# Kernel tuning notes

Hardware: AMD Instinct MI355X
Metric: run time of the kernel (lower is better)

The kernel has to match this reference:

```python
import jax, jax.numpy as jnp
import numpy as np

B, S, D, H, F = 4, 2048, 1024, 16, 4096
HD = D // H
NEG = -2.0 ** 32
EPS = 1e-5


def _gelu(x):
    return x * 0.5 * (1.0 + jax.scipy.special.erf(x / jnp.sqrt(2.0).astype(x.dtype)))


def _layernorm(x, scale, offset):
    mu = jnp.mean(x, axis=-1, keepdims=True)
    var = jnp.mean(jnp.square(x - mu), axis=-1, keepdims=True)
    return (x - mu) * jax.lax.rsqrt(var + EPS) * scale + offset


def setup_inputs() -> dict:
    key = jax.random.key(0)
    ks = jax.random.split(key, 12)
    s = 0.02
    return {
        "x": jax.random.normal(ks[0], (B, S, D), jnp.float32),
        "mask": jnp.zeros((B, S), jnp.int32),  # 1 = masked-out (padding)
        "Wq": jax.random.normal(ks[1], (D, D), jnp.float32) * s,
        "bq": jnp.zeros((D,), jnp.float32),
        "Wk": jax.random.normal(ks[2], (D, D), jnp.float32) * s,
        "bk": jnp.zeros((D,), jnp.float32),
        "Wv": jax.random.normal(ks[3], (D, D), jnp.float32) * s,
        "bv": jnp.zeros((D,), jnp.float32),
        "Wo": jax.random.normal(ks[4], (D, D), jnp.float32) * s,
        "bo": jnp.zeros((D,), jnp.float32),
        "ln1_s": jnp.ones((D,), jnp.float32),
        "ln1_b": jnp.zeros((D,), jnp.float32),
        "W1": jax.random.normal(ks[5], (D, F), jnp.float32) * s,
        "b1": jnp.zeros((F,), jnp.float32),
        "W2": jax.random.normal(ks[6], (F, D), jnp.float32) * s,
        "b2": jnp.zeros((D,), jnp.float32),
        "ln2_s": jnp.ones((D,), jnp.float32),
        "ln2_b": jnp.zeros((D,), jnp.float32),
    }


def reference(x, mask, Wq, bq, Wk, bk, Wv, bv, Wo, bo, ln1_s, ln1_b,
              W1, b1, W2, b2, ln2_s, ln2_b):
    b, s, d = x.shape
    q = (x @ Wq + bq).reshape(b, s, H, HD)
    k = (x @ Wk + bk).reshape(b, s, H, HD)
    v = (x @ Wv + bv).reshape(b, s, H, HD)
    logits = jnp.einsum('btnh,bsnh->bnts', q, k) / jnp.sqrt(jnp.float32(HD))
    logits = logits + (mask.astype(jnp.float32) * NEG)[:, None, None, :]
    attn = jax.nn.softmax(logits, axis=-1)
    ctx = jnp.einsum('bsnh,bnts->btnh', v, attn).reshape(b, s, d)
    attn_out = ctx @ Wo + bo
    h = _layernorm(attn_out + x, ln1_s, ln1_b)
    mlp = _gelu(h @ W1 + b1) @ W2 + b2
    return _layernorm(mlp + h, ln2_s, ln2_b)
```

## Files before the change

kernel.cpp:

```cpp
#include <hip/hip_runtime.h>
#include <hip/hip_bf16.h>

typedef __attribute__((ext_vector_type(8))) short short8;
typedef __attribute__((ext_vector_type(4))) short s16x4;
typedef __attribute__((ext_vector_type(4))) float f32x4;
typedef unsigned short u16;

#define DEV __device__ __forceinline__
#define MFMA32(a, b, c) __builtin_amdgcn_mfma_f32_16x16x32_bf16(a, b, c, 0, 0, 0)
#define MFMA16(a, b, c) __builtin_amdgcn_mfma_f32_16x16x16bf16_1k(a, b, c, 0, 0, 0)

DEV u16 f2b(float f) {
    __hip_bfloat16 h = __float2bfloat16(f);
    return __builtin_bit_cast(unsigned short, h);
}

DEV float max3f(float a, float b, float c) {
    float d;
    asm("v_max3_f32 %0, %1, %2, %3" : "=v"(d) : "v"(a), "v"(b), "v"(c));
    return d;
}

DEV void gl_lds16(const u16* g, u16* l) {
    __builtin_amdgcn_global_load_lds((const unsigned int*)g, (unsigned int*)l, 16, 0, 0);
}

__global__ __launch_bounds__(256) void cast_bf16(const float* __restrict__ in, u16* __restrict__ out, int n) {
    int i = (blockIdx.x * 256 + threadIdx.x) * 4;
    if (i < n) {
        float4 v = *(const float4*)(in + i);
        ushort4 o;
        o.x = f2b(v.x); o.y = f2b(v.y); o.z = f2b(v.z); o.w = f2b(v.w);
        *(ushort4*)(out + i) = o;
    }
}

__global__ __launch_bounds__(256) void transpose_cast(const float* __restrict__ in, u16* __restrict__ out,
                                                      int R, int C) {
    __shared__ float t[32][33];
    int bx = blockIdx.x * 32;
    int by = blockIdx.y * 32;
    int tx = threadIdx.x, ty = threadIdx.y;
#pragma unroll
    for (int i = 0; i < 32; i += 8) t[ty + i][tx] = in[(size_t)(by + ty + i) * C + bx + tx];
    __syncthreads();
#pragma unroll
    for (int i = 0; i < 32; i += 8) out[(size_t)(bx + ty + i) * R + by + tx] = f2b(t[tx][ty + i]);
}

__global__ __launch_bounds__(256) void pack_bias(const float* __restrict__ bq, const float* __restrict__ bk,
                                                 const float* __restrict__ bv, const float* __restrict__ bo,
                                                 const float* __restrict__ b1, const float* __restrict__ b2,
                                                 float* __restrict__ out) {
    int i = blockIdx.x * 256 + threadIdx.x;
    if (i >= 9216) return;
    float v;
    if (i < 1024) v = bq[i];
    else if (i < 2048) v = bk[i - 1024];
    else if (i < 3072) v = bv[i - 2048];
    else if (i < 4096) v = bo[i - 3072];
    else if (i < 8192) v = b1[i - 4096];
    else v = b2[i - 8192];
    out[i] = v;
}

template <bool GELU, bool BF16OUT, bool RESID>
__global__ __launch_bounds__(256) void gemm_bt(const u16* __restrict__ A, const u16* __restrict__ B,
                                               const float* __restrict__ bias, float* __restrict__ cf,
                                               u16* __restrict__ cb, const float* __restrict__ res,
                                               int M, int N, int K) {
    __shared__ __align__(16) u16 As[128 * 32];
    __shared__ __align__(16) u16 Bs[128 * 32];
    const int tid = threadIdx.x;
    const int wid = tid >> 6, lane = tid & 63;
    const int wr = wid >> 1, wc = wid & 1;
    const int m0 = blockIdx.x * 128, n0 = blockIdx.y * 128;
    const int r16 = lane & 15, g = lane >> 4;
    const int lrow = lane >> 2, lk = (lane & 3) * 8;

    f32x4 acc[4][4];
#pragma unroll
    for (int i = 0; i < 4; i++)
#pragma unroll
        for (int j = 0; j < 4; j++) acc[i][j] = (f32x4){0.f, 0.f, 0.f, 0.f};

    const u16* ga = A + (size_t)(m0 + wid * 32 + lrow) * K + lk;
    const u16* gb = B + (size_t)(n0 + wid * 32 + lrow) * K + lk;
    u16* lA0 = &As[(wid * 32) * 32];
    u16* lA1 = &As[(wid * 32 + 16) * 32];
    u16* lB0 = &Bs[(wid * 32) * 32];
    u16* lB1 = &Bs[(wid * 32 + 16) * 32];

    for (int kt = 0; kt < K; kt += 32) {
        gl_lds16(ga + kt, lA0);
        gl_lds16(ga + (size_t)16 * K + kt, lA1);
        gl_lds16(gb + kt, lB0);
        gl_lds16(gb + (size_t)16 * K + kt, lB1);
        __syncthreads();
        short8 af[4], bfr[4];
#pragma unroll
        for (int i = 0; i < 4; i++) af[i] = *(const short8*)&As[(wr * 64 + i * 16 + r16) * 32 + g * 8];
#pragma unroll
        for (int j = 0; j < 4; j++) bfr[j] = *(const short8*)&Bs[(wc * 64 + j * 16 + r16) * 32 + g * 8];
#pragma unroll
        for (int i = 0; i < 4; i++)
#pragma unroll
            for (int j = 0; j < 4; j++) acc[i][j] = MFMA32(af[i], bfr[j], acc[i][j]);
        __syncthreads();
    }

#pragma unroll
    for (int i = 0; i < 4; i++) {
#pragma unroll
        for (int j = 0; j < 4; j++) {
#pragma unroll
            for (int r = 0; r < 4; r++) {
                int row = m0 + wr * 64 + i * 16 + g * 4 + r;
                int col = n0 + wc * 64 + j * 16 + r16;
                float v = acc[i][j][r] + bias[col];
                if (RESID) v += res[(size_t)row * N + col];
                if (GELU) v = 0.5f * v * (1.0f + erff(v * 0.70710678118654752f));
                if (BF16OUT) cb[(size_t)row * N + col] = f2b(v);
                else cf[(size_t)row * N + col] = v;
            }
        }
    }
}

__global__ __launch_bounds__(256, 4) void attn_kernel(const u16* __restrict__ qkv, const int* __restrict__ mask,
                                                      u16* __restrict__ ctx) {
    const int tid = threadIdx.x, wid = tid >> 6, lane = tid & 63;
    const int r16 = lane & 15, g = lane >> 4;
    const int h = blockIdx.y, b = blockIdx.z;
    const size_t baserow = (size_t)b * 2048;
    const int q0 = blockIdx.x * 128;

    __shared__ __align__(16) u16 Ks[64 * 64];
    __shared__ __align__(16) u16 Vs[64 * 64];
    __shared__ unsigned tflags_sh;

    const float SCALE = 0.18033688011112042f;
    const float MNEG = -6.196328018e9f;
    const s16x4 ONES = {(short)0x3F80, (short)0x3F80, (short)0x3F80, (short)0x3F80};

    short8 qfA0, qfA1, qfB0, qfB1;
    {
        const u16* qp = qkv + (baserow + q0 + wid * 32 + r16) * 3072 + h * 64 + g * 8;
        qfA0 = *(const short8*)qp;
        qfA1 = *(const short8*)(qp + 32);
        qfB0 = *(const short8*)(qp + (size_t)16 * 3072);
        qfB1 = *(const short8*)(qp + (size_t)16 * 3072 + 32);
    }

    if (tid == 0) tflags_sh = 0;
    __syncthreads();
    for (int r = 0; r < 8; ++r) {
        int v = mask[baserow + r * 256 + tid];
        unsigned long long bal = __ballot(v != 0);
        if (bal != 0 && lane == 0) atomicOr(&tflags_sh, 1u << (r * 4 + wid));
    }

    const int L = lane;
    const u16* kg0 = qkv + (baserow + wid * 16 + (L >> 3)) * 3072 + 1024 + h * 64 + ((L & 7) ^ (L >> 3)) * 8;
    const u16* kg1 = kg0 + (size_t)8 * 3072;
    u16* kl0 = &Ks[wid * 1024];
    u16* kl1 = &Ks[wid * 1024 + 512];
    const u16* vg0 = qkv + (baserow + wid * 16 + ((L & 31) >> 1)) * 3072 + 2048 + h * 64
                     + ((L >> 5) * 16 + (L & 1) * 8);
    const u16* vg1 = vg0 + 32;
    u16* vl0 = &Vs[wid * 1024];
    u16* vl1 = &Vs[wid * 1024 + 512];
    const unsigned vaddr = (unsigned)(unsigned long long)&Vs[0] + (unsigned)(r16 * 2 + g * 128);

    __syncthreads();
    const unsigned tfl = tflags_sh;

    f32x4 OtA[4], OtB[4];
#pragma unroll
    for (int dt = 0; dt < 4; dt++) { OtA[dt] = (f32x4){0.f, 0.f, 0.f, 0.f}; OtB[dt] = (f32x4){0.f, 0.f, 0.f, 0.f}; }
    f32x4 OsumA = (f32x4){0.f, 0.f, 0.f, 0.f}, OsumB = (f32x4){0.f, 0.f, 0.f, 0.f};
    float mrunA = -1e30f, mrunB = -1e30f;

    for (int t = 0; t < 32; ++t) {
        const int kt = t * 64;
        const size_t go = (size_t)kt * 3072;
        gl_lds16(kg0 + go, kl0);
        gl_lds16(kg1 + go, kl1);
        gl_lds16(vg0 + go, vl0);
        gl_lds16(vg1 + go, vl1);
        __syncthreads();

        f32x4 zA[4], zB[4];
        __builtin_amdgcn_s_setprio(1);
#pragma unroll
        for (int tt = 0; tt < 4; tt++) {
            const int row = tt * 16 + r16;
            const int swz = row & 7;
            short8 a0 = *(const short8*)&Ks[row * 64 + ((g ^ swz) * 8)];
            short8 a1 = *(const short8*)&Ks[row * 64 + (((4 + g) ^ swz) * 8)];
            f32x4 za = (f32x4){0.f, 0.f, 0.f, 0.f};
            za = MFMA32(a0, qfA0, za);
            za = MFMA32(a1, qfA1, za);
            zA[tt] = za;
            f32x4 zb = (f32x4){0.f, 0.f, 0.f, 0.f};
            zb = MFMA32(a0, qfB0, zb);
            zb = MFMA32(a1, qfB1, zb);
            zB[tt] = zb;
        }
        __builtin_amdgcn_s_setprio(0);

        float a0_ = max3f(zA[0][0], zA[0][1], zA[0][2]);
        float a1_ = max3f(zA[0][3], zA[1][0], zA[1][1]);
        float a2_ = max3f(zA[1][2], zA[1][3], zA[2][0]);
        float a3_ = max3f(zA[2][1], zA[2][2], zA[2][3]);
        float a4_ = max3f(zA[3][0], zA[3][1], zA[3][2]);
        float zmaxA = fmaxf(max3f(a0_, a1_, a2_), max3f(a3_, a4_, zA[3][3]));
        float b0_ = max3f(zB[0][0], zB[0][1], zB[0][2]);
        float b1_ = max3f(zB[0][3], zB[1][0], zB[1][1]);
        float b2_ = max3f(zB[1][2], zB[1][3], zB[2][0]);
        float b3_ = max3f(zB[2][1], zB[2][2], zB[2][3]);
        float b4_ = max3f(zB[3][0], zB[3][1], zB[3][2]);
        float zmaxB = fmaxf(max3f(b0_, b1_, b2_), max3f(b3_, b4_, zB[3][3]));
        zmaxA = fmaxf(zmaxA, __shfl_xor(zmaxA, 16));
        zmaxB = fmaxf(zmaxB, __shfl_xor(zmaxB, 16));
        zmaxA = fmaxf(zmaxA, __shfl_xor(zmaxA, 32));
        zmaxB = fmaxf(zmaxB, __shfl_xor(zmaxB, 32));
        float pmaxA = zmaxA * SCALE, pmaxB = zmaxB * SCALE;

        if (!__all(pmaxA - mrunA <= 11.5f)) {
            float mnew = fmaxf(mrunA, pmaxA);
            float alpha = exp2f(mrunA - mnew);
            mrunA = mnew;
            OsumA *= alpha;
#pragma unroll
            for (int dt = 0; dt < 4; dt++) OtA[dt] *= alpha;
        }
        if (!__all(pmaxB - mrunB <= 11.5f)) {
            float mnew = fmaxf(mrunB, pmaxB);
            float alpha = exp2f(mrunB - mnew);
            mrunB = mnew;
            OsumB *= alpha;
#pragma unroll
            for (int dt = 0; dt < 4; dt++) OtB[dt] *= alpha;
        }

        s16x4 pbA[4], pbB[4];
        const float negmA = -mrunA, negmB = -mrunB;
        if (__builtin_expect((tfl >> t) & 1u, 0)) {
            const int* mrow = mask + baserow + kt;
#pragma unroll
            for (int tt = 0; tt < 4; tt++) {
                float pa[4], pbv[4];
#pragma unroll
                for (int j = 0; j < 4; j++) {
                    float mbj = mrow[tt * 16 + g * 4 + j] ? MNEG : 0.0f;
                    pa[j] = exp2f(__builtin_fmaf(zA[tt][j], SCALE, mbj + negmA));
                    pbv[j] = exp2f(__builtin_fmaf(zB[tt][j], SCALE, mbj + negmB));
                }
                unsigned lo, hi;
                asm("v_cvt_pk_bf16_f32 %0, %1, %2" : "=v"(lo) : "v"(pa[0]), "v"(pa[1]));
                asm("v_cvt_pk_bf16_f32 %0, %1, %2" : "=v"(hi) : "v"(pa[2]), "v"(pa[3]));
                uint2 ua; ua.x = lo; ua.y = hi;
                pbA[tt] = __builtin_bit_cast(s16x4, ua);
                asm("v_cvt_pk_bf16_f32 %0, %1, %2" : "=v"(lo) : "v"(pbv[0]), "v"(pbv[1]));
                asm("v_cvt_pk_bf16_f32 %0, %1, %2" : "=v"(hi) : "v"(pbv[2]), "v"(pbv[3]));
                uint2 ub; ub.x = lo; ub.y = hi;
                pbB[tt] = __builtin_bit_cast(s16x4, ub);
            }
        } else {
#pragma unroll
            for (int tt = 0; tt < 4; tt++) {
                float pa0 = exp2f(__builtin_fmaf(zA[tt][0], SCALE, negmA));
                float pa1 = exp2f(__builtin_fmaf(zA[tt][1], SCALE, negmA));
                float pa2 = exp2f(__builtin_fmaf(zA[tt][2], SCALE, negmA));
                float pa3 = exp2f(__builtin_fmaf(zA[tt][3], SCALE, negmA));
                float pb0 = exp2f(__builtin_fmaf(zB[tt][0], SCALE, negmB));
                float pb1 = exp2f(__builtin_fmaf(zB[tt][1], SCALE, negmB));
                float pb2 = exp2f(__builtin_fmaf(zB[tt][2], SCALE, negmB));
                float pb3 = exp2f(__builtin_fmaf(zB[tt][3], SCALE, negmB));
                unsigned lo, hi;
                asm("v_cvt_pk_bf16_f32 %0, %1, %2" : "=v"(lo) : "v"(pa0), "v"(pa1));
                asm("v_cvt_pk_bf16_f32 %0, %1, %2" : "=v"(hi) : "v"(pa2), "v"(pa3));
                uint2 ua; ua.x = lo; ua.y = hi;
                pbA[tt] = __builtin_bit_cast(s16x4, ua);
                asm("v_cvt_pk_bf16_f32 %0, %1, %2" : "=v"(lo) : "v"(pb0), "v"(pb1));
                asm("v_cvt_pk_bf16_f32 %0, %1, %2" : "=v"(hi) : "v"(pb2), "v"(pb3));
                uint2 ub; ub.x = lo; ub.y = hi;
                pbB[tt] = __builtin_bit_cast(s16x4, ub);
            }
        }

        s16x4 vf[2][4];
#pragma unroll
        for (int dt = 0; dt < 4; dt++)
            asm volatile("ds_read_b64_tr_b16 %0, %1"
                         : "=v"(vf[0][dt]) : "v"(vaddr + (unsigned)(dt * 512)));
#pragma unroll
        for (int tt = 0; tt < 4; tt++) {
            if (tt < 3) {
#pragma unroll
                for (int dt = 0; dt < 4; dt++)
                    asm volatile("ds_read_b64_tr_b16 %0, %1"
                                 : "=v"(vf[(tt + 1) & 1][dt])
                                 : "v"(vaddr + (unsigned)(((tt + 1) * 4 + dt) * 512)));
                asm volatile("s_waitcnt lgkmcnt(4)" ::: "memory");
            } else {
                asm volatile("s_waitcnt lgkmcnt(0)" ::: "memory");
            }
            __builtin_amdgcn_sched_barrier(0);
            __builtin_amdgcn_s_setprio(1);
#pragma unroll
            for (int dt = 0; dt < 4; dt++) {
                OtA[dt] = MFMA16(vf[tt & 1][dt], pbA[tt], OtA[dt]);
                OtB[dt] = MFMA16(vf[tt & 1][dt], pbB[tt], OtB[dt]);
            }
            OsumA = MFMA16(ONES, pbA[tt], OsumA);
            OsumB = MFMA16(ONES, pbB[tt], OsumB);
            __builtin_amdgcn_s_setprio(0);
        }
        __syncthreads();
    }

    const float rlA = 1.0f / OsumA[0];
    const float rlB = 1.0f / OsumB[0];
    u16* cpA = ctx + (baserow + q0 + wid * 32 + r16) * 1024 + h * 64 + g * 4;
    u16* cpB = cpA + (size_t)16 * 1024;
#pragma unroll
    for (int dt = 0; dt < 4; dt++) {
        ushort4 oa, ob;
        oa.x = f2b(OtA[dt][0] * rlA); oa.y = f2b(OtA[dt][1] * rlA);
        oa.z = f2b(OtA[dt][2] * rlA); oa.w = f2b(OtA[dt][3] * rlA);
        ob.x = f2b(OtB[dt][0] * rlB); ob.y = f2b(OtB[dt][1] * rlB);
        ob.z = f2b(OtB[dt][2] * rlB); ob.w = f2b(OtB[dt][3] * rlB);
        *(ushort4*)(cpA + dt * 16) = oa;
        *(ushort4*)(cpB + dt * 16) = ob;
    }
}

__global__ __launch_bounds__(256) void ln_kernel(const float* __restrict__ a, const float* __restrict__ res,
                                                 const float* __restrict__ gamma, const float* __restrict__ beta,
                                                 float* __restrict__ outf, u16* __restrict__ outb) {
    const int row = blockIdx.x, tid = threadIdx.x;
    const size_t base = (size_t)row * 1024 + tid * 4;
    float4 va = *(const float4*)(a + base);
    float x0 = va.x, x1 = va.y, x2 = va.z, x3 = va.w;
    if (res) {
        float4 vr = *(const float4*)(res + base);
        x0 += vr.x; x1 += vr.y; x2 += vr.z; x3 += vr.w;
    }
    float s = x0 + x1 + x2 + x3;
    float ss = x0 * x0 + x1 * x1 + x2 * x2 + x3 * x3;
#pragma unroll
    for (int m = 1; m < 64; m <<= 1) { s += __shfl_xor(s, m, 64); ss += __shfl_xor(ss, m, 64); }
    __shared__ float red[8];
    if ((tid & 63) == 0) { red[tid >> 6] = s; red[4 + (tid >> 6)] = ss; }
    __syncthreads();
    s = red[0] + red[1] + red[2] + red[3];
    ss = red[4] + red[5] + red[6] + red[7];
    float mu = s * (1.0f / 1024.0f);
    float var = ss * (1.0f / 1024.0f) - mu * mu;
    float rstd = rsqrtf(var + 1e-5f);
    float4 g4 = *(const float4*)(gamma + tid * 4);
    float4 b4 = *(const float4*)(beta + tid * 4);
    float y0 = (x0 - mu) * rstd * g4.x + b4.x;
    float y1 = (x1 - mu) * rstd * g4.y + b4.y;
    float y2 = (x2 - mu) * rstd * g4.z + b4.z;
    float y3 = (x3 - mu) * rstd * g4.w + b4.w;
    *(float4*)(outf + base) = make_float4(y0, y1, y2, y3);
    if (outb) {
        ushort4 ob;
        ob.x = f2b(y0); ob.y = f2b(y1); ob.z = f2b(y2); ob.w = f2b(y3);
        *(ushort4*)(outb + base) = ob;
    }
}

extern "C" void kernel_launch(void* const* d_in, const int* in_sizes, int n_in, void* d_out, int out_size,
                              void* d_ws, size_t ws_size, hipStream_t stream) {
    const float* x = (const float*)d_in[0];
    const int* mask = (const int*)d_in[1];
    const float* Wq = (const float*)d_in[2];
    const float* bq = (const float*)d_in[3];
    const float* Wk = (const float*)d_in[4];
    const float* bk = (const float*)d_in[5];
    const float* Wv = (const float*)d_in[6];
    const float* bv = (const float*)d_in[7];
    const float* Wo = (const float*)d_in[8];
    const float* bo = (const float*)d_in[9];
    const float* ln1s = (const float*)d_in[10];
    const float* ln1b = (const float*)d_in[11];
    const float* W1 = (const float*)d_in[12];
    const float* b1 = (const float*)d_in[13];
    const float* W2 = (const float*)d_in[14];
    const float* b2 = (const float*)d_in[15];
    const float* ln2s = (const float*)d_in[16];
    const float* ln2b = (const float*)d_in[17];
    float* out = (float*)d_out;
    char* ws = (char*)d_ws;

    const size_t MB = 1024 * 1024;
    u16* XB = (u16*)(ws + 0);
    u16* WTq = (u16*)(ws + 16 * MB);
    u16* WTk = WTq + 1024 * 1024;
    u16* WTv = WTk + 1024 * 1024;
    u16* WTo = WTv + 1024 * 1024;
    u16* WT1 = WTo + 1024 * 1024;
    u16* WT2 = WT1 + 4096 * 1024;
    float* BIAS = (float*)(ws + 40 * MB);
    u16* QKV = (u16*)(ws + 41 * MB);
    u16* CTX = (u16*)(ws + 0);
    float* ATT = (float*)(ws + 41 * MB);
    float* Hbuf = (float*)(ws + 73 * MB);
    u16* HB = (u16*)(ws + 105 * MB);
    u16* MLP1 = (u16*)(ws + 121 * MB);
    float* MLP2 = (float*)(ws + 41 * MB);

    dim3 tb(32, 8);
    cast_bf16<<<8192, 256, 0, stream>>>(x, XB, 8192 * 1024);
    transpose_cast<<<dim3(32, 32), tb, 0, stream>>>(Wq, WTq, 1024, 1024);
    transpose_cast<<<dim3(32, 32), tb, 0, stream>>>(Wk, WTk, 1024, 1024);
    transpose_cast<<<dim3(32, 32), tb, 0, stream>>>(Wv, WTv, 1024, 1024);
    transpose_cast<<<dim3(32, 32), tb, 0, stream>>>(Wo, WTo, 1024, 1024);
    transpose_cast<<<dim3(128, 32), tb, 0, stream>>>(W1, WT1, 1024, 4096);
    transpose_cast<<<dim3(32, 128), tb, 0, stream>>>(W2, WT2, 4096, 1024);
    pack_bias<<<36, 256, 0, stream>>>(bq, bk, bv, bo, b1, b2, BIAS);

    gemm_bt<false, true, false><<<dim3(64, 24), 256, 0, stream>>>(XB, WTq, BIAS, nullptr, QKV, nullptr, 8192, 3072, 1024);
    attn_kernel<<<dim3(16, 16, 4), 256, 0, stream>>>(QKV, mask, CTX);
    gemm_bt<false, false, true><<<dim3(64, 8), 256, 0, stream>>>(CTX, WTo, BIAS + 3072, ATT, nullptr, x, 8192, 1024, 1024);
    ln_kernel<<<8192, 256, 0, stream>>>(ATT, nullptr, ln1s, ln1b, Hbuf, HB);
    gemm_bt<true, true, false><<<dim3(64, 32), 256, 0, stream>>>(HB, WT1, BIAS + 4096, nullptr, MLP1, nullptr, 8192, 4096, 1024);
    gemm_bt<false, false, true><<<dim3(64, 8), 256, 0, stream>>>(MLP1, WT2, BIAS + 8192, MLP2, nullptr, Hbuf, 8192, 1024, 4096);
    ln_kernel<<<8192, 256, 0, stream>>>(MLP2, nullptr, ln2s, ln2b, out, nullptr);
}
```

Baseline: 518.3 us.

## Double GEMM K-tile to 64 and XOR-swizzle LDS layout

The bf16 GEMM now stages a K depth of 64 per iteration instead of 32, which halves the number of barrier pairs per K sweep. Each thread loads 16-byte chunks whose column position is XOR-swizzled by row. The fragment reads undo the same swizzle, which is meant to avoid LDS bank conflicts on the wider 128-byte rows. LDS use per block doubles to 32 KB, which may lower occupancy, and there is still no double buffering.

```diff
diff --git a/kernel.cpp b/kernel.cpp
--- a/kernel.cpp
+++ b/kernel.cpp
@@ -69,14 +69,14 @@
                                                const float* __restrict__ bias, float* __restrict__ cf,
                                                u16* __restrict__ cb, const float* __restrict__ res,
                                                int M, int N, int K) {
-    __shared__ __align__(16) u16 As[128 * 32];
-    __shared__ __align__(16) u16 Bs[128 * 32];
+    __shared__ __align__(16) u16 As[128 * 64];
+    __shared__ __align__(16) u16 Bs[128 * 64];
     const int tid = threadIdx.x;
     const int wid = tid >> 6, lane = tid & 63;
     const int wr = wid >> 1, wc = wid & 1;
     const int m0 = blockIdx.x * 128, n0 = blockIdx.y * 128;
     const int r16 = lane & 15, g = lane >> 4;
-    const int lrow = lane >> 2, lk = (lane & 3) * 8;
+    const int sw = r16 & 7;
 
     f32x4 acc[4][4];
 #pragma unroll
@@ -84,28 +84,36 @@
 #pragma unroll
         for (int j = 0; j < 4; j++) acc[i][j] = (f32x4){0.f, 0.f, 0.f, 0.f};
 
-    const u16* ga = A + (size_t)(m0 + wid * 32 + lrow) * K + lk;
-    const u16* gb = B + (size_t)(n0 + wid * 32 + lrow) * K + lk;
-    u16* lA0 = &As[(wid * 32) * 32];
-    u16* lA1 = &As[(wid * 32 + 16) * 32];
-    u16* lB0 = &Bs[(wid * 32) * 32];
-    u16* lB1 = &Bs[(wid * 32 + 16) * 32];
-
-    for (int kt = 0; kt < K; kt += 32) {
-        gl_lds16(ga + kt, lA0);
-        gl_lds16(ga + (size_t)16 * K + kt, lA1);
-        gl_lds16(gb + kt, lB0);
-        gl_lds16(gb + (size_t)16 * K + kt, lB1);
+    const int srow = tid >> 3;
+    const int schunk = (tid & 7) ^ (srow & 7);
+    const u16* ga = A + (size_t)(m0 + srow) * K + schunk * 8;
+    const u16* gb = B + (size_t)(n0 + srow) * K + schunk * 8;
+
+    for (int kt = 0; kt < K; kt += 64) {
+#pragma unroll
+        for (int j = 0; j < 4; j++) {
+            gl_lds16(ga + (size_t)(j * 32) * K + kt, &As[(j * 32 + wid * 8) * 64]);
+            gl_lds16(gb + (size_t)(j * 32) * K + kt, &Bs[(j * 32 + wid * 8) * 64]);
+        }
         __syncthreads();
-        short8 af[4], bfr[4];
-#pragma unroll
-        for (int i = 0; i < 4; i++) af[i] = *(const short8*)&As[(wr * 64 + i * 16 + r16) * 32 + g * 8];
-#pragma unroll
-        for (int j = 0; j < 4; j++) bfr[j] = *(const short8*)&Bs[(wc * 64 + j * 16 + r16) * 32 + g * 8];
-#pragma unroll
-        for (int i = 0; i < 4; i++)
-#pragma unroll
-            for (int j = 0; j < 4; j++) acc[i][j] = MFMA32(af[i], bfr[j], acc[i][j]);
+#pragma unroll
+        for (int ks = 0; ks < 2; ks++) {
+            short8 af[4], bfr[4];
+#pragma unroll
+            for (int i = 0; i < 4; i++) {
+                int row = wr * 64 + i * 16 + r16;
+                af[i] = *(const short8*)((const char*)As + row * 128 + (((ks * 4 + g) ^ sw) * 16));
+            }
+#pragma unroll
+            for (int j = 0; j < 4; j++) {
+                int row = wc * 64 + j * 16 + r16;
+                bfr[j] = *(const short8*)((const char*)Bs + row * 128 + (((ks * 4 + g) ^ sw) * 16));
+            }
+#pragma unroll
+            for (int i = 0; i < 4; i++)
+#pragma unroll
+                for (int j = 0; j < 4; j++) acc[i][j] = MFMA32(af[i], bfr[j], acc[i][j]);
+        }
         __syncthreads();
     }
 
```

After: 486.1 us. -6.2%, faster.
